# Kernel tuning notes

Measured on AMD Instinct MI355X. Metric: run time of the kernel, lower is better.

The kernel has to match this reference:

```python
import jax, jax.numpy as jnp
import numpy as np

INPUT_DIM = 128
HIDDEN_DIM = 256
TOP_K = 512
M = 8192
N = 8192


def setup_inputs() -> dict:
    key = jax.random.key(0)
    ks = jax.random.split(key, 10)
    s_in = 1.0 / np.sqrt(INPUT_DIM)
    s_h = 1.0 / np.sqrt(HIDDEN_DIM)
    return {
        "desc0": jax.random.normal(ks[0], (1, M, INPUT_DIM), jnp.float32),
        "desc1": jax.random.normal(ks[1], (1, N, INPUT_DIM), jnp.float32),
        # mlpc0: Linear(in,h) -> ReLU -> Linear(h,h); weights stored [in,out]
        "W0a": jax.random.uniform(ks[2], (INPUT_DIM, HIDDEN_DIM), jnp.float32, -s_in, s_in),
        "b0a": jax.random.uniform(ks[3], (HIDDEN_DIM,), jnp.float32, -s_in, s_in),
        "W0b": jax.random.uniform(ks[4], (HIDDEN_DIM, HIDDEN_DIM), jnp.float32, -s_h, s_h),
        "b0b": jax.random.uniform(ks[5], (HIDDEN_DIM,), jnp.float32, -s_h, s_h),
        "W1a": jax.random.uniform(ks[6], (INPUT_DIM, HIDDEN_DIM), jnp.float32, -s_in, s_in),
        "b1a": jax.random.uniform(ks[7], (HIDDEN_DIM,), jnp.float32, -s_in, s_in),
        "W1b": jax.random.uniform(ks[8], (HIDDEN_DIM, HIDDEN_DIM), jnp.float32, -s_h, s_h),
        "b1b": jax.random.uniform(ks[9], (HIDDEN_DIM,), jnp.float32, -s_h, s_h),
    }


def _mlp(x, Wa, ba, Wb, bb):
    h = jax.nn.relu(x @ Wa + ba)
    return h @ Wb + bb


def reference(desc0, desc1, W0a, b0a, W0b, b0b, W1a, b1a, W1b, b1b):
    mdesc0 = _mlp(desc0, W0a, b0a, W0b, b0b)  # [1, M, H]
    mdesc1 = _mlp(desc1, W1a, b1a, W1b, b1b)  # [1, N, H]
    sim = jnp.einsum("bmd,bnd->bmn", mdesc0, mdesc1)  # [1, M, N]
    flat = sim[0].reshape(-1)
    _, top_idx = jax.lax.top_k(flat, TOP_K)
    n = sim.shape[2]
    rows = top_idx // n
    cols = top_idx % n
    top_k_indices_2d = jnp.stack([rows, cols], axis=1)  # [TOP_K, 2]
    return top_k_indices_2d, sim
```

## Files before the change

### kernel.cpp

```cpp
#include <hip/hip_runtime.h>
#include <stdint.h>

#define H_DIM 256
#define NCOL 8192
#define TOPK 512
#define CAND_CAP 8192

typedef unsigned short u16;
typedef __attribute__((ext_vector_type(8))) __bf16 bf16x8;
typedef __attribute__((ext_vector_type(4))) float f32x4;
typedef unsigned __attribute__((address_space(3))) lds_u32;
typedef const unsigned __attribute__((address_space(1))) glb_u32;

__device__ __forceinline__ unsigned fkey(float f) {
  unsigned u = __float_as_uint(f);
  unsigned m = (unsigned)((int)u >> 31) | 0x80000000u;
  return u ^ m;
}

__device__ __forceinline__ u16 f2bf_rne(float f) {
  unsigned u = __float_as_uint(f);
  return (u16)((u + 0x7fffu + ((u >> 16) & 1u)) >> 16);
}

__device__ __forceinline__ float bf2f(u16 h) {
  return __uint_as_float(((unsigned)h) << 16);
}

__global__ __launch_bounds__(256) void zero_ws(unsigned* __restrict__ ghist,
                                               unsigned* __restrict__ counter) {
  int t = blockIdx.x * blockDim.x + threadIdx.x;
  if (t < 4096) ghist[t] = 0;
  if (t == 0) *counter = 0;
}

template <int K, bool RELU, bool EMIT>
__global__ __launch_bounds__(256) void mlp_layer(const float* __restrict__ X,
                                                 const float* __restrict__ W,
                                                 const float* __restrict__ bias,
                                                 float* __restrict__ Y,
                                                 u16* __restrict__ hi,
                                                 u16* __restrict__ lo) {
  __shared__ float Xs[16 * K];
  const int t = threadIdx.x;
  const int row0 = blockIdx.x * 16;
  for (int f = t; f < 4 * K; f += 256) {
    *(float4*)(Xs + f * 4) = *(const float4*)(X + (size_t)row0 * K + f * 4);
  }
  __syncthreads();
  const int cg = (t & 63) * 4;
  const int rg = (t >> 6) * 4;
  float acc[4][4];
#pragma unroll
  for (int r = 0; r < 4; r++)
#pragma unroll
    for (int c = 0; c < 4; c++) acc[r][c] = 0.f;

  for (int d = 0; d < K; d += 4) {
    float4 w0 = *(const float4*)(W + (d + 0) * H_DIM + cg);
    float4 w1 = *(const float4*)(W + (d + 1) * H_DIM + cg);
    float4 w2 = *(const float4*)(W + (d + 2) * H_DIM + cg);
    float4 w3 = *(const float4*)(W + (d + 3) * H_DIM + cg);
#pragma unroll
    for (int r = 0; r < 4; r++) {
      float4 x = *(const float4*)(Xs + (rg + r) * K + d);
#pragma unroll
      for (int c = 0; c < 4; c++) {
        float a = acc[r][c];
        a = fmaf(x.x, ((const float*)&w0)[c], a);
        a = fmaf(x.y, ((const float*)&w1)[c], a);
        a = fmaf(x.z, ((const float*)&w2)[c], a);
        a = fmaf(x.w, ((const float*)&w3)[c], a);
        acc[r][c] = a;
      }
    }
  }
  const float4 bv = *(const float4*)(bias + cg);
#pragma unroll
  for (int r = 0; r < 4; r++) {
    float4 v;
    v.x = acc[r][0] + bv.x;
    v.y = acc[r][1] + bv.y;
    v.z = acc[r][2] + bv.z;
    v.w = acc[r][3] + bv.w;
    if (RELU) {
      v.x = fmaxf(v.x, 0.f);
      v.y = fmaxf(v.y, 0.f);
      v.z = fmaxf(v.z, 0.f);
      v.w = fmaxf(v.w, 0.f);
    }
    const size_t grow = (size_t)(row0 + rg + r);
    *(float4*)(Y + grow * H_DIM + cg) = v;
    if (EMIT) {
      ushort4 hv, lv;
      hv.x = f2bf_rne(v.x); lv.x = f2bf_rne(v.x - bf2f(hv.x));
      hv.y = f2bf_rne(v.y); lv.y = f2bf_rne(v.y - bf2f(hv.y));
      hv.z = f2bf_rne(v.z); lv.z = f2bf_rne(v.z - bf2f(hv.z));
      hv.w = f2bf_rne(v.w); lv.w = f2bf_rne(v.w - bf2f(hv.w));
      *(ushort4*)(hi + grow * H_DIM + cg) = hv;
      *(ushort4*)(lo + grow * H_DIM + cg) = lv;
    }
  }
}

__global__ __launch_bounds__(512, 2) void gemm_sim_mfma(const u16* __restrict__ Ah,
                                                        const u16* __restrict__ Al,
                                                        const u16* __restrict__ Bh,
                                                        const u16* __restrict__ Bl,
                                                        float* __restrict__ C,
                                                        unsigned* __restrict__ ghist) {
  __shared__ __align__(16) char SB[131072];
  const int t = threadIdx.x;
  const int wave = t >> 6, lane = t & 63;
  const int wm = wave >> 2, wn = wave & 3;
  const int bid = blockIdx.x;
  const int swz = (bid & 7) * 128 + (bid >> 3);
  const int m0 = (swz >> 5) * 256, n0 = (swz & 31) * 256;

  f32x4 acc[8][4];
#pragma unroll
  for (int i = 0; i < 8; i++)
#pragma unroll
    for (int j = 0; j < 4; j++) acc[i][j] = (f32x4){0.f, 0.f, 0.f, 0.f};

  const int srow = t >> 3;
  const int scolE = ((t & 7) ^ (srow & 7)) << 3;
  const int lrow = lane & 15;
  const int kq16 = (lane >> 4) << 4;
  const int asz = (lrow & 7) << 4;

  auto STAGE = [&](int bsel, int tt) {
    const u16* pa = (tt < 8) ? Ah : Al;
    const u16* pb = (tt < 4) ? Bh : ((tt < 8) ? Bl : Bh);
    const int kofs = (tt & 3) * 64;
    char* base = SB + bsel * 65536;
    const size_t aoff = (size_t)(m0 + srow) * H_DIM + kofs + scolE;
    const size_t boff = (size_t)(n0 + srow) * H_DIM + kofs + scolE;
#pragma unroll
    for (int i = 0; i < 4; i++)
      __builtin_amdgcn_global_load_lds((glb_u32*)(pa + aoff + (size_t)i * 64 * H_DIM),
                                       (lds_u32*)(base + i * 8192 + wave * 1024), 16, 0, 0);
#pragma unroll
    for (int i = 0; i < 4; i++)
      __builtin_amdgcn_global_load_lds((glb_u32*)(pb + boff + (size_t)i * 64 * H_DIM),
                                       (lds_u32*)(base + 32768 + i * 8192 + wave * 1024), 16, 0, 0);
  };

  STAGE(0, 0);
  for (int tt = 0; tt < 12; ++tt) {
    if (tt + 1 < 12) {
      STAGE((tt + 1) & 1, tt + 1);
      asm volatile("s_waitcnt vmcnt(8)" ::: "memory");
    } else {
      asm volatile("s_waitcnt vmcnt(0)" ::: "memory");
    }
    __builtin_amdgcn_s_barrier();
    asm volatile("" ::: "memory");
    const char* bb = SB + (tt & 1) * 65536;
#pragma unroll
    for (int kk = 0; kk < 2; ++kk) {
      bf16x8 af[8], bfr[4];
#pragma unroll
      for (int fm = 0; fm < 8; fm++)
        af[fm] = *(const bf16x8*)(bb + (wm * 128 + fm * 16 + lrow) * 128 +
                                  ((kk * 64 + kq16) ^ asz));
#pragma unroll
      for (int fn = 0; fn < 4; fn++)
        bfr[fn] = *(const bf16x8*)(bb + 32768 + (wn * 64 + fn * 16 + lrow) * 128 +
                                   ((kk * 64 + kq16) ^ asz));
      __builtin_amdgcn_s_setprio(1);
#pragma unroll
      for (int fm = 0; fm < 8; fm++)
#pragma unroll
        for (int fn = 0; fn < 4; fn++)
          acc[fm][fn] =
              __builtin_amdgcn_mfma_f32_16x16x32_bf16(af[fm], bfr[fn], acc[fm][fn], 0, 0, 0);
      __builtin_amdgcn_s_setprio(0);
    }
    __builtin_amdgcn_s_barrier();
    asm volatile("" ::: "memory");
  }

  unsigned* hist = (unsigned*)SB;
  float* Ct = (float*)(SB + 16384);
  for (int i = t; i < 4096; i += 512) hist[i] = 0;
  __syncthreads();
#pragma unroll
  for (int ch = 0; ch < 4; ++ch) {
    if (wm == (ch >> 1)) {
      const int fmb = (ch & 1) * 4;
#pragma unroll
      for (int fi = 0; fi < 4; fi++)
#pragma unroll
        for (int fn = 0; fn < 4; fn++)
#pragma unroll
          for (int q = 0; q < 4; q++)
            Ct[(fi * 16 + (lane >> 4) * 4 + q) * 260 + wn * 64 + fn * 16 + lrow] =
                acc[fmb + fi][fn][q];
    }
    __syncthreads();
#pragma unroll
    for (int u = 0; u < 8; ++u) {
      const int idx = t + u * 512;
      const int row = idx >> 6, c4 = idx & 63;
      float4 v = *(const float4*)(Ct + row * 260 + c4 * 4);
      *(float4*)(C + (size_t)(m0 + ch * 64 + row) * NCOL + n0 + c4 * 4) = v;
      atomicAdd(&hist[fkey(v.x) >> 20], 1u);
      atomicAdd(&hist[fkey(v.y) >> 20], 1u);
      atomicAdd(&hist[fkey(v.z) >> 20], 1u);
      atomicAdd(&hist[fkey(v.w) >> 20], 1u);
    }
    __syncthreads();
  }
  for (int bq = t; bq < 4096; bq += 512) {
    unsigned cc = hist[bq];
    if (cc) atomicAdd(&ghist[bq], cc);
  }
}

__global__ __launch_bounds__(256) void find_thresh(const unsigned* __restrict__ ghist,
                                                   unsigned* __restrict__ thresh) {
  __shared__ unsigned part[256];
  const int t = threadIdx.x;
  unsigned s = 0;
#pragma unroll
  for (int b = 0; b < 16; b++) s += ghist[t * 16 + b];
  part[t] = s;
  __syncthreads();
  if (t == 0) {
    unsigned cum = 0;
    int g = 255;
    for (; g > 0; g--) {
      if (cum + part[g] >= TOPK) break;
      cum += part[g];
    }
    int bsel = g * 16;
    for (int b = g * 16 + 15; b >= g * 16; b--) {
      cum += ghist[b];
      if (cum >= TOPK) { bsel = b; break; }
    }
    *thresh = (unsigned)bsel << 20;
  }
}

__device__ __forceinline__ void cand_push(unsigned kapprox, unsigned thr_m, unsigned idx,
                                          const float* __restrict__ m0f,
                                          const float* __restrict__ m1f,
                                          unsigned long long* __restrict__ cand,
                                          unsigned* __restrict__ counter) {
  if (kapprox >= thr_m) {
    const unsigned row = idx >> 13;
    const unsigned col = idx & 8191u;
    const float4* a4 = (const float4*)(m0f + (size_t)row * H_DIM);
    const float4* b4 = (const float4*)(m1f + (size_t)col * H_DIM);
    float v = 0.f;
#pragma unroll 8
    for (int k = 0; k < H_DIM / 4; k++) {
      float4 a = a4[k], b = b4[k];
      v = fmaf(a.x, b.x, v);
      v = fmaf(a.y, b.y, v);
      v = fmaf(a.z, b.z, v);
      v = fmaf(a.w, b.w, v);
    }
    unsigned p = atomicAdd(counter, 1u);
    if (p < CAND_CAP)
      cand[p] = ((unsigned long long)fkey(v) << 32) |
                (unsigned long long)(0xFFFFFFFFu - idx);
  }
}

__global__ __launch_bounds__(256) void collect(const float* __restrict__ sim,
                                               const unsigned* __restrict__ thresh,
                                               const float* __restrict__ m0f,
                                               const float* __restrict__ m1f,
                                               unsigned long long* __restrict__ cand,
                                               unsigned* __restrict__ counter) {
  const unsigned thr = *thresh;
  const unsigned thr_m = thr > 4096u ? thr - 4096u : 0u;
  const int stride = gridDim.x * blockDim.x;
  const int total4 = (NCOL * NCOL) / 4;
  const float4* s4 = (const float4*)sim;
  for (int i = blockIdx.x * blockDim.x + threadIdx.x; i < total4; i += stride) {
    float4 v = s4[i];
    unsigned base = (unsigned)i * 4u;
    cand_push(fkey(v.x), thr_m, base + 0u, m0f, m1f, cand, counter);
    cand_push(fkey(v.y), thr_m, base + 1u, m0f, m1f, cand, counter);
    cand_push(fkey(v.z), thr_m, base + 2u, m0f, m1f, cand, counter);
    cand_push(fkey(v.w), thr_m, base + 3u, m0f, m1f, cand, counter);
  }
}

__global__ __launch_bounds__(1024) void sort_topk(const unsigned long long* __restrict__ cand,
                                                  const unsigned* __restrict__ counter,
                                                  float* __restrict__ out) {
  __shared__ unsigned long long s[CAND_CAP];
  const int t = threadIdx.x;
  int n = (int)min(*counter, (unsigned)CAND_CAP);
  int P = 512;
  while (P < n) P <<= 1;
  for (int i = t; i < P; i += 1024) s[i] = (i < n) ? cand[i] : 0ULL;
  __syncthreads();
  for (int k = 2; k <= P; k <<= 1) {
    for (int j = k >> 1; j > 0; j >>= 1) {
      for (int i = t; i < P; i += 1024) {
        int l = i ^ j;
        if (l > i) {
          bool desc = ((i & k) == 0);
          unsigned long long a = s[i], b = s[l];
          bool sw = desc ? (a < b) : (a > b);
          if (sw) { s[i] = b; s[l] = a; }
        }
      }
      __syncthreads();
    }
  }
  if (t < TOPK) {
    unsigned long long c = s[t];
    unsigned idx = 0xFFFFFFFFu - (unsigned)(c & 0xFFFFFFFFull);
    unsigned row = idx >> 13;
    unsigned col = idx & 8191u;
    out[t * 2 + 0] = (float)row;
    out[t * 2 + 1] = (float)col;
  }
}

extern "C" void kernel_launch(void* const* d_in, const int* in_sizes, int n_in,
                              void* d_out, int out_size, void* d_ws, size_t ws_size,
                              hipStream_t stream) {
  const float* desc0 = (const float*)d_in[0];
  const float* desc1 = (const float*)d_in[1];
  const float* W0a = (const float*)d_in[2];
  const float* b0a = (const float*)d_in[3];
  const float* W0b = (const float*)d_in[4];
  const float* b0b = (const float*)d_in[5];
  const float* W1a = (const float*)d_in[6];
  const float* b1a = (const float*)d_in[7];
  const float* W1b = (const float*)d_in[8];
  const float* b1b = (const float*)d_in[9];

  char* ws = (char*)d_ws;
  unsigned* ghist = (unsigned*)ws;
  unsigned* counter = (unsigned*)(ws + 16384);
  unsigned* thresh = (unsigned*)(ws + 16388);
  unsigned long long* cand = (unsigned long long*)(ws + 16448);
  float* mdesc0f = (float*)(ws + 131072);
  float* mdesc1f = mdesc0f + 8192 * 256;
  float* hbuf = mdesc1f + 8192 * 256;
  u16* Ahh = (u16*)(hbuf + 8192 * 256);
  u16* All = Ahh + 8192 * 256;
  u16* Bhh = All + 8192 * 256;
  u16* Bll = Bhh + 8192 * 256;

  float* outf = (float*)d_out;
  float* sim = outf + TOPK * 2;

  zero_ws<<<16, 256, 0, stream>>>(ghist, counter);

  mlp_layer<128, true, false><<<512, 256, 0, stream>>>(desc0, W0a, b0a, hbuf, nullptr, nullptr);
  mlp_layer<256, false, true><<<512, 256, 0, stream>>>(hbuf, W0b, b0b, mdesc0f, Ahh, All);
  mlp_layer<128, true, false><<<512, 256, 0, stream>>>(desc1, W1a, b1a, hbuf, nullptr, nullptr);
  mlp_layer<256, false, true><<<512, 256, 0, stream>>>(hbuf, W1b, b1b, mdesc1f, Bhh, Bll);

  gemm_sim_mfma<<<1024, 512, 0, stream>>>(Ahh, All, Bhh, Bll, sim, ghist);
  find_thresh<<<1, 256, 0, stream>>>(ghist, thresh);
  collect<<<4096, 256, 0, stream>>>(sim, thresh, mdesc0f, mdesc1f, cand, counter);
  sort_topk<<<1, 1024, 0, stream>>>(cand, counter, outf);
}
```

Measured before the change: 659.2 us.

## Batch MLP launches, restage split-bf16 GEMM, and radix-select candidates before sorting

Merges the zeroing kernel and the two pairs of MLP layer launches into two dual-input launches with separate hidden buffers, so there are fewer launches and more blocks in flight. The similarity GEMM now stages the hi and lo halves of each K slice together and runs three MFMA passes (hi*hi, hi*lo, lo*hi) per slice in 8 iterations instead of 12, which cuts redundant reloads. The top-k sort replaces a bitonic sort over up to 8192 candidates with a bitwise radix select that finds the 512th key, then bitonic-sorts only 512 entries. The radix select costs 64 barrier rounds, and ties at the threshold key are resolved by arrival order.

New measurement: 568.4 us. -13.8%, faster.

```diff
diff --git a/kernel.cpp b/kernel.cpp
--- a/kernel.cpp
+++ b/kernel.cpp
@@ -27,23 +27,30 @@
   return __uint_as_float(((unsigned)h) << 16);
 }
 
-__global__ __launch_bounds__(256) void zero_ws(unsigned* __restrict__ ghist,
-                                               unsigned* __restrict__ counter) {
-  int t = blockIdx.x * blockDim.x + threadIdx.x;
-  if (t < 4096) ghist[t] = 0;
-  if (t == 0) *counter = 0;
-}
-
-template <int K, bool RELU, bool EMIT>
-__global__ __launch_bounds__(256) void mlp_layer(const float* __restrict__ X,
-                                                 const float* __restrict__ W,
-                                                 const float* __restrict__ bias,
-                                                 float* __restrict__ Y,
-                                                 u16* __restrict__ hi,
-                                                 u16* __restrict__ lo) {
+template <int K, bool RELU, bool EMIT, bool ZERO>
+__global__ __launch_bounds__(256) void mlp_dual(
+    const float* __restrict__ X0, const float* __restrict__ W0,
+    const float* __restrict__ bias0, float* __restrict__ Y0,
+    u16* __restrict__ h0, u16* __restrict__ l0,
+    const float* __restrict__ X1, const float* __restrict__ W1,
+    const float* __restrict__ bias1, float* __restrict__ Y1,
+    u16* __restrict__ h1, u16* __restrict__ l1,
+    unsigned* __restrict__ ghist, unsigned* __restrict__ counter) {
   __shared__ float Xs[16 * K];
   const int t = threadIdx.x;
-  const int row0 = blockIdx.x * 16;
+  if (ZERO && blockIdx.x == 0) {
+    for (int i = t; i < 4096; i += 256) ghist[i] = 0;
+    if (t == 0) *counter = 0;
+  }
+  const int half = blockIdx.x >> 9;
+  const float* X = half ? X1 : X0;
+  const float* W = half ? W1 : W0;
+  const float* bias = half ? bias1 : bias0;
+  float* Y = half ? Y1 : Y0;
+  u16* hi = half ? h1 : h0;
+  u16* lo = half ? l1 : l0;
+  const int row0 = (blockIdx.x & 511) * 16;
+
   for (int f = t; f < 4 * K; f += 256) {
     *(float4*)(Xs + f * 4) = *(const float4*)(X + (size_t)row0 * K + f * 4);
   }
@@ -123,32 +130,35 @@
 #pragma unroll
     for (int j = 0; j < 4; j++) acc[i][j] = (f32x4){0.f, 0.f, 0.f, 0.f};
 
-  const int srow = t >> 3;
-  const int scolE = ((t & 7) ^ (srow & 7)) << 3;
+  const int srow8 = t >> 3;
+  const int sA = (t & 7) ^ (srow8 & 7);
+  const u16* pAsrc = (sA < 4) ? Ah : Al;
+  const u16* pBsrc = (sA < 4) ? Bh : Bl;
+  const int scolE = (sA & 3) * 8;
   const int lrow = lane & 15;
   const int kq16 = (lane >> 4) << 4;
   const int asz = (lrow & 7) << 4;
+  const int cH = kq16 ^ asz;
+  const int cL = (64 + kq16) ^ asz;
 
   auto STAGE = [&](int bsel, int tt) {
-    const u16* pa = (tt < 8) ? Ah : Al;
-    const u16* pb = (tt < 4) ? Bh : ((tt < 8) ? Bl : Bh);
-    const int kofs = (tt & 3) * 64;
+    const int kofs = tt * 32;
     char* base = SB + bsel * 65536;
-    const size_t aoff = (size_t)(m0 + srow) * H_DIM + kofs + scolE;
-    const size_t boff = (size_t)(n0 + srow) * H_DIM + kofs + scolE;
+    const size_t ar = (size_t)(m0 + srow8) * H_DIM + kofs + scolE;
+    const size_t br = (size_t)(n0 + srow8) * H_DIM + kofs + scolE;
 #pragma unroll
     for (int i = 0; i < 4; i++)
-      __builtin_amdgcn_global_load_lds((glb_u32*)(pa + aoff + (size_t)i * 64 * H_DIM),
+      __builtin_amdgcn_global_load_lds((glb_u32*)(pAsrc + ar + (size_t)i * 64 * H_DIM),
                                        (lds_u32*)(base + i * 8192 + wave * 1024), 16, 0, 0);
 #pragma unroll
     for (int i = 0; i < 4; i++)
-      __builtin_amdgcn_global_load_lds((glb_u32*)(pb + boff + (size_t)i * 64 * H_DIM),
+      __builtin_amdgcn_global_load_lds((glb_u32*)(pBsrc + br + (size_t)i * 64 * H_DIM),
                                        (lds_u32*)(base + 32768 + i * 8192 + wave * 1024), 16, 0, 0);
   };
 
   STAGE(0, 0);
-  for (int tt = 0; tt < 12; ++tt) {
-    if (tt + 1 < 12) {
+  for (int tt = 0; tt < 8; ++tt) {
+    if (tt < 7) {
       STAGE((tt + 1) & 1, tt + 1);
       asm volatile("s_waitcnt vmcnt(8)" ::: "memory");
     } else {
@@ -157,24 +167,42 @@
     __builtin_amdgcn_s_barrier();
     asm volatile("" ::: "memory");
     const char* bb = SB + (tt & 1) * 65536;
-#pragma unroll
-    for (int kk = 0; kk < 2; ++kk) {
-      bf16x8 af[8], bfr[4];
+    const char* bA = bb + (wm * 128 + lrow) * 128;
+    const char* bB = bb + 32768 + (wn * 64 + lrow) * 128;
+    bf16x8 aH[8], bH[4];
+#pragma unroll
+    for (int fm = 0; fm < 8; fm++) aH[fm] = *(const bf16x8*)(bA + fm * 2048 + cH);
+#pragma unroll
+    for (int fn = 0; fn < 4; fn++) bH[fn] = *(const bf16x8*)(bB + fn * 2048 + cH);
+    __builtin_amdgcn_s_setprio(1);
+#pragma unroll
+    for (int fm = 0; fm < 8; fm++)
+#pragma unroll
+      for (int fn = 0; fn < 4; fn++)
+        acc[fm][fn] = __builtin_amdgcn_mfma_f32_16x16x32_bf16(aH[fm], bH[fn], acc[fm][fn], 0, 0, 0);
+    __builtin_amdgcn_s_setprio(0);
+    {
+      bf16x8 bL[4];
+#pragma unroll
+      for (int fn = 0; fn < 4; fn++) bL[fn] = *(const bf16x8*)(bB + fn * 2048 + cL);
+      __builtin_amdgcn_s_setprio(1);
 #pragma unroll
       for (int fm = 0; fm < 8; fm++)
-        af[fm] = *(const bf16x8*)(bb + (wm * 128 + fm * 16 + lrow) * 128 +
-                                  ((kk * 64 + kq16) ^ asz));
-#pragma unroll
-      for (int fn = 0; fn < 4; fn++)
-        bfr[fn] = *(const bf16x8*)(bb + 32768 + (wn * 64 + fn * 16 + lrow) * 128 +
-                                   ((kk * 64 + kq16) ^ asz));
+#pragma unroll
+        for (int fn = 0; fn < 4; fn++)
+          acc[fm][fn] = __builtin_amdgcn_mfma_f32_16x16x32_bf16(aH[fm], bL[fn], acc[fm][fn], 0, 0, 0);
+      __builtin_amdgcn_s_setprio(0);
+    }
+    {
+      bf16x8 aL[8];
+#pragma unroll
+      for (int fm = 0; fm < 8; fm++) aL[fm] = *(const bf16x8*)(bA + fm * 2048 + cL);
       __builtin_amdgcn_s_setprio(1);
 #pragma unroll
       for (int fm = 0; fm < 8; fm++)
 #pragma unroll
         for (int fn = 0; fn < 4; fn++)
-          acc[fm][fn] =
-              __builtin_amdgcn_mfma_f32_16x16x32_bf16(af[fm], bfr[fn], acc[fm][fn], 0, 0, 0);
+          acc[fm][fn] = __builtin_amdgcn_mfma_f32_16x16x32_bf16(aL[fm], bH[fn], acc[fm][fn], 0, 0, 0);
       __builtin_amdgcn_s_setprio(0);
     }
     __builtin_amdgcn_s_barrier();
@@ -293,34 +321,64 @@
 __global__ __launch_bounds__(1024) void sort_topk(const unsigned long long* __restrict__ cand,
                                                   const unsigned* __restrict__ counter,
                                                   float* __restrict__ out) {
-  __shared__ unsigned long long s[CAND_CAP];
+  __shared__ unsigned long long top[TOPK];
+  __shared__ unsigned wred[16];
+  __shared__ unsigned long long pfx_sh;
+  __shared__ unsigned cnt_sh;
   const int t = threadIdx.x;
-  int n = (int)min(*counter, (unsigned)CAND_CAP);
-  int P = 512;
-  while (P < n) P <<= 1;
-  for (int i = t; i < P; i += 1024) s[i] = (i < n) ? cand[i] : 0ULL;
+  const int n = (int)min(*counter, (unsigned)CAND_CAP);
+  unsigned long long e[CAND_CAP / 1024];
+#pragma unroll
+  for (int u = 0; u < CAND_CAP / 1024; ++u) {
+    const int i = t + u * 1024;
+    e[u] = (i < n) ? cand[i] : 0ULL;
+  }
+  if (t == 0) cnt_sh = 0;
   __syncthreads();
-  for (int k = 2; k <= P; k <<= 1) {
+  unsigned long long pfx = 0;
+  for (int b = 63; b >= 0; --b) {
+    const unsigned long long q = pfx | (1ULL << b);
+    unsigned c = 0;
+#pragma unroll
+    for (int u = 0; u < CAND_CAP / 1024; ++u) c += (e[u] >= q) ? 1u : 0u;
+#pragma unroll
+    for (int off = 32; off; off >>= 1) c += __shfl_down(c, off, 64);
+    if ((t & 63) == 0) wred[t >> 6] = c;
+    __syncthreads();
+    if (t == 0) {
+      unsigned tot = 0;
+#pragma unroll
+      for (int w = 0; w < 16; ++w) tot += wred[w];
+      pfx_sh = (tot >= TOPK) ? q : pfx;
+    }
+    __syncthreads();
+    pfx = pfx_sh;
+  }
+#pragma unroll
+  for (int u = 0; u < CAND_CAP / 1024; ++u) {
+    if (e[u] >= pfx) {
+      unsigned p = atomicAdd(&cnt_sh, 1u);
+      if (p < TOPK) top[p] = e[u];
+    }
+  }
+  __syncthreads();
+  for (int k = 2; k <= TOPK; k <<= 1) {
     for (int j = k >> 1; j > 0; j >>= 1) {
-      for (int i = t; i < P; i += 1024) {
-        int l = i ^ j;
-        if (l > i) {
-          bool desc = ((i & k) == 0);
-          unsigned long long a = s[i], b = s[l];
-          bool sw = desc ? (a < b) : (a > b);
-          if (sw) { s[i] = b; s[l] = a; }
+      if (t < TOPK) {
+        const int l = t ^ j;
+        if (l > t) {
+          const bool desc = ((t & k) == 0);
+          unsigned long long a = top[t], b2 = top[l];
+          if (desc ? (a < b2) : (a > b2)) { top[t] = b2; top[l] = a; }
         }
       }
       __syncthreads();
     }
   }
   if (t < TOPK) {
-    unsigned long long c = s[t];
-    unsigned idx = 0xFFFFFFFFu - (unsigned)(c & 0xFFFFFFFFull);
-    unsigned row = idx >> 13;
-    unsigned col = idx & 8191u;
-    out[t * 2 + 0] = (float)row;
-    out[t * 2 + 1] = (float)col;
+    const unsigned idx = 0xFFFFFFFFu - (unsigned)(top[t] & 0xFFFFFFFFull);
+    out[t * 2 + 0] = (float)(idx >> 13);
+    out[t * 2 + 1] = (float)(idx & 8191u);
   }
 }
 
@@ -345,8 +403,9 @@
   unsigned long long* cand = (unsigned long long*)(ws + 16448);
   float* mdesc0f = (float*)(ws + 131072);
   float* mdesc1f = mdesc0f + 8192 * 256;
-  float* hbuf = mdesc1f + 8192 * 256;
-  u16* Ahh = (u16*)(hbuf + 8192 * 256);
+  float* hbuf0 = mdesc1f + 8192 * 256;
+  float* hbuf1 = hbuf0 + 8192 * 256;
+  u16* Ahh = (u16*)(hbuf1 + 8192 * 256);
   u16* All = Ahh + 8192 * 256;
   u16* Bhh = All + 8192 * 256;
   u16* Bll = Bhh + 8192 * 256;
@@ -354,12 +413,12 @@
   float* outf = (float*)d_out;
   float* sim = outf + TOPK * 2;
 
-  zero_ws<<<16, 256, 0, stream>>>(ghist, counter);
-
-  mlp_layer<128, true, false><<<512, 256, 0, stream>>>(desc0, W0a, b0a, hbuf, nullptr, nullptr);
-  mlp_layer<256, false, true><<<512, 256, 0, stream>>>(hbuf, W0b, b0b, mdesc0f, Ahh, All);
-  mlp_layer<128, true, false><<<512, 256, 0, stream>>>(desc1, W1a, b1a, hbuf, nullptr, nullptr);
-  mlp_layer<256, false, true><<<512, 256, 0, stream>>>(hbuf, W1b, b1b, mdesc1f, Bhh, Bll);
+  mlp_dual<128, true, false, true><<<1024, 256, 0, stream>>>(
+      desc0, W0a, b0a, hbuf0, nullptr, nullptr,
+      desc1, W1a, b1a, hbuf1, nullptr, nullptr, ghist, counter);
+  mlp_dual<256, false, true, false><<<1024, 256, 0, stream>>>(
+      hbuf0, W0b, b0b, mdesc0f, Ahh, All,
+      hbuf1, W1b, b1b, mdesc1f, Bhh, Bll, ghist, counter);
 
   gemm_sim_mfma<<<1024, 512, 0, stream>>>(Ahh, All, Bhh, Bll, sim, ghist);
   find_thresh<<<1, 256, 0, stream>>>(ghist, thresh);
```
